# Performance work log

Hardware: AMD Instinct MI355X
Metric: run time of the kernel (lower is better)

## Reference

```python
import jax, jax.numpy as jnp
import numpy as np

B, H, KVH, HD, S = 16, 32, 8, 128, 4096
D = H * HD  # 4096
Q = 1  # decode: one query token per batch element


def rotate_half(x):
    half = x.shape[-1] // 2
    return jnp.concatenate([-x[..., half:], x[..., :half]], axis=-1)


def setup_inputs() -> dict:
    key = jax.random.key(0)
    ks = jax.random.split(key, 8)
    hidden_states = jax.random.normal(ks[0], (B, Q, D), dtype=jnp.float32)
    current_steps = jax.random.randint(ks[1], (B,), 0, S - 1)
    # additive causal mask per batch: positions <= current_step visible
    pos = jnp.arange(S)[None, :]
    attention_mask = jnp.where(pos <= current_steps[:, None], 0.0, -1e9).astype(jnp.float32)[:, None, None, :]  # [B,1,1,S]
    # RoPE cos/sin at each batch element's current position
    inv_freq = 1.0 / (10000.0 ** (jnp.arange(0, HD, 2, dtype=jnp.float32) / HD))
    ang = current_steps[:, None].astype(jnp.float32) * inv_freq[None, :]  # [B, HD/2]
    ang = jnp.concatenate([ang, ang], axis=-1)  # [B, HD]
    cos = jnp.cos(ang)[:, None, None, :]  # [B,1,1,HD]
    sin = jnp.sin(ang)[:, None, None, :]
    past_key = jax.random.normal(ks[2], (B, KVH, S, HD), dtype=jnp.float32)
    past_value = jax.random.normal(ks[3], (B, KVH, S, HD), dtype=jnp.float32)
    sc = 1.0 / np.sqrt(D)
    Wq = jax.random.normal(ks[4], (D, H * HD), dtype=jnp.float32) * sc
    Wk = jax.random.normal(ks[5], (D, KVH * HD), dtype=jnp.float32) * sc
    Wv = jax.random.normal(ks[6], (D, KVH * HD), dtype=jnp.float32) * sc
    Wo = jax.random.normal(ks[7], (H * HD, D), dtype=jnp.float32) * sc
    return dict(hidden_states=hidden_states, attention_mask=attention_mask,
                current_steps=current_steps, cos=cos, sin=sin,
                past_key=past_key, past_value=past_value,
                Wq=Wq, Wk=Wk, Wv=Wv, Wo=Wo)


def reference(hidden_states, attention_mask, current_steps, cos, sin,
              past_key, past_value, Wq, Wk, Wv, Wo):
    b, q_len, d = hidden_states.shape
    # projections -> [B, heads, Q, HD]
    q = (hidden_states @ Wq).reshape(b, q_len, H, HD).transpose(0, 2, 1, 3)
    k = (hidden_states @ Wk).reshape(b, q_len, KVH, HD).transpose(0, 2, 1, 3)
    v = (hidden_states @ Wv).reshape(b, q_len, KVH, HD).transpose(0, 2, 1, 3)
    # RoPE
    q = q * cos + rotate_half(q) * sin
    k = k * cos + rotate_half(k) * sin
    # KV-cache scatter at current_step per batch (slice_scatter equivalent)
    def upd(cache_b, new_b, step):
        return jax.lax.dynamic_update_slice(cache_b, new_b, (0, step, 0))
    new_key = jax.vmap(upd)(past_key, k, current_steps)      # [B,KVH,S,HD]
    new_value = jax.vmap(upd)(past_value, v, current_steps)  # [B,KVH,S,HD]
    # GQA attention
    g = H // KVH
    qg = q.reshape(b, KVH, g, q_len, HD)
    scores = jnp.einsum('bkgqd,bksd->bkgqs', qg, new_key) / np.sqrt(HD)
    scores = scores + attention_mask[:, :, None, :, :]  # [B,1,1,Q,S] broadcast
    probs = jax.nn.softmax(scores, axis=-1)
    out = jnp.einsum('bkgqs,bksd->bkgqd', probs, new_value)
    out = out.reshape(b, H, q_len, HD).transpose(0, 2, 1, 3).reshape(b, q_len, H * HD)
    attn_out = out @ Wo
    return attn_out, new_key, new_value
```

## Files before the change

kernel.cpp:

```cpp
#include <hip/hip_runtime.h>

#define B 16
#define H 32
#define KVH 8
#define HD 128
#define S 4096
#define D 4096
#define NQKV 6144
#define PSPLIT 32
#define WSPLIT 32
#define NCH 16
#define CROWS (S / NCH)
#define SCALE 0.08838834764831845f

typedef float nfloat4 __attribute__((ext_vector_type(4)));

__device__ __forceinline__ float4 ntload4(const float4* p) {
  nfloat4 r = __builtin_nontemporal_load(reinterpret_cast<const nfloat4*>(p));
  return *reinterpret_cast<float4*>(&r);
}
__device__ __forceinline__ float ntloadf(const float* p) {
  return __builtin_nontemporal_load(p);
}

__global__ void k_proj(const float* __restrict__ hs, const float* __restrict__ Wq,
                       const float* __restrict__ Wk, const float* __restrict__ Wv,
                       float* __restrict__ part) {
  __shared__ float4 hsT[D / PSPLIT][4];
  int t = threadIdx.x;
  int n = blockIdx.x * 256 + t;
  int k0 = blockIdx.y * (D / PSPLIT);
#pragma unroll
  for (int i = 0; i < (D / PSPLIT) * 4 / 256; i++) {
    int idx = i * 256 + t;
    int k = idx >> 2, b4 = idx & 3;
    hsT[k][b4] = make_float4(hs[(size_t)(b4 * 4 + 0) * D + k0 + k],
                             hs[(size_t)(b4 * 4 + 1) * D + k0 + k],
                             hs[(size_t)(b4 * 4 + 2) * D + k0 + k],
                             hs[(size_t)(b4 * 4 + 3) * D + k0 + k]);
  }
  const float* w; int ldw, col;
  if (n < 4096)      { w = Wq; ldw = 4096; col = n; }
  else if (n < 5120) { w = Wk; ldw = 1024; col = n - 4096; }
  else               { w = Wv; ldw = 1024; col = n - 5120; }
  float acc[B];
#pragma unroll
  for (int b = 0; b < B; b++) acc[b] = 0.f;
  const float* wp = w + (size_t)k0 * ldw + col;
  __syncthreads();
#pragma unroll 4
  for (int k = 0; k < D / PSPLIT; k++) {
    float wv = ntloadf(&wp[(size_t)k * ldw]);
    float4 h0 = hsT[k][0], h1 = hsT[k][1], h2 = hsT[k][2], h3 = hsT[k][3];
    acc[0]  = fmaf(h0.x, wv, acc[0]);  acc[1]  = fmaf(h0.y, wv, acc[1]);
    acc[2]  = fmaf(h0.z, wv, acc[2]);  acc[3]  = fmaf(h0.w, wv, acc[3]);
    acc[4]  = fmaf(h1.x, wv, acc[4]);  acc[5]  = fmaf(h1.y, wv, acc[5]);
    acc[6]  = fmaf(h1.z, wv, acc[6]);  acc[7]  = fmaf(h1.w, wv, acc[7]);
    acc[8]  = fmaf(h2.x, wv, acc[8]);  acc[9]  = fmaf(h2.y, wv, acc[9]);
    acc[10] = fmaf(h2.z, wv, acc[10]); acc[11] = fmaf(h2.w, wv, acc[11]);
    acc[12] = fmaf(h3.x, wv, acc[12]); acc[13] = fmaf(h3.y, wv, acc[13]);
    acc[14] = fmaf(h3.z, wv, acc[14]); acc[15] = fmaf(h3.w, wv, acc[15]);
  }
  float* p = part + (size_t)blockIdx.y * (B * NQKV);
#pragma unroll
  for (int b = 0; b < B; b++) p[(size_t)b * NQKV + n] = acc[b];
}

__global__ void k_reduce_rope(const float* __restrict__ part, const float* __restrict__ cosb,
                              const float* __restrict__ sinb, const int* __restrict__ steps,
                              float* __restrict__ qr, float* __restrict__ nkrow,
                              float* __restrict__ nvrow) {
  int i = blockIdx.x * 256 + threadIdx.x;
  int b = i / 3584, n2 = i % 3584;
  if (n2 < 2560) {
    int hr = n2 >> 6, d = n2 & 63;
    int n_lo = hr * 128 + d, n_hi = n_lo + 64;
    float vlo = 0.f, vhi = 0.f;
#pragma unroll
    for (int c = 0; c < PSPLIT; c++) {
      const float* pc = part + (size_t)c * B * NQKV + (size_t)b * NQKV;
      vlo += ntloadf(&pc[n_lo]);
      vhi += ntloadf(&pc[n_hi]);
    }
    float clo = cosb[b * HD + d], chi = cosb[b * HD + d + 64];
    float slo = sinb[b * HD + d], shi = sinb[b * HD + d + 64];
    float rlo = vlo * clo - vhi * slo;
    float rhi = vhi * chi + vlo * shi;
    if (n_lo < 4096) {
      qr[(size_t)b * D + n_lo] = rlo;
      qr[(size_t)b * D + n_hi] = rhi;
    } else {
      nkrow[(size_t)b * KVH * HD + (n_lo - 4096)] = rlo;
      nkrow[(size_t)b * KVH * HD + (n_hi - 4096)] = rhi;
    }
  } else {
    int j = n2 - 2560;
    float v = 0.f;
#pragma unroll
    for (int c = 0; c < PSPLIT; c++)
      v += ntloadf(&part[(size_t)c * B * NQKV + (size_t)b * NQKV + 5120 + j]);
    nvrow[(size_t)b * KVH * HD + j] = v;
  }
}

__global__ void __launch_bounds__(256)
k_flashKV(const float* __restrict__ pastk, const float* __restrict__ pastv,
          const float* __restrict__ nkrow, const float* __restrict__ nvrow,
          const float* __restrict__ qr, const int* __restrict__ steps,
          float* __restrict__ newk, float* __restrict__ newv,
          float* __restrict__ part, float* __restrict__ stats) {
  int ch = blockIdx.x, kvh = blockIdx.y, b = blockIdx.z;
  int t = threadIdx.x;
  __shared__ float sbuf[CROWS][4];
  __shared__ float redmx[4][4];
  __shared__ float redsm[4][4];
  __shared__ float4 red4[4][4][32];
  int s0 = ch * CROWS;
  int step = steps[b];
  int L = step + 1;
  int h0 = kvh * 4;
  bool any = (s0 < L);
  int w = t >> 6;
  int d4 = t & 31, rr = t >> 5;

  const float4* srcv = (const float4*)(pastv + ((size_t)(b * KVH + kvh) * S + s0) * HD);
  float4*       dstv = (float4*)(newv + ((size_t)(b * KVH + kvh) * S + s0) * HD);
  float4 vsub = ((const float4*)(nvrow + (size_t)(b * KVH + kvh) * HD))[d4];

  {
    int ln = t & 15, rg = t >> 4;
    const float4* qbase = (const float4*)(qr + ((size_t)b * H + h0) * HD);
    float4 q0[4], q1[4];
#pragma unroll
    for (int h = 0; h < 4; h++) {
      q0[h] = qbase[h * 32 + ln];
      q1[h] = qbase[h * 32 + ln + 16];
    }
    const float4* subp = (const float4*)(nkrow + (size_t)(b * KVH + kvh) * HD);
    float4 sub0 = subp[ln], sub1 = subp[ln + 16];
    const float4* src = (const float4*)(pastk + ((size_t)(b * KVH + kvh) * S + s0) * HD);
    float4*       dst = (float4*)(newk + ((size_t)(b * KVH + kvh) * S + s0) * HD);
#pragma unroll 4
    for (int it = 0; it < CROWS / 16; ++it) {
      int row = it * 16 + rg;
      size_t o0 = (size_t)row * 32 + ln;
      float4 k0 = ntload4(&src[o0]);
      float4 k1 = ntload4(&src[o0 + 16]);
      if (s0 + row == step) { k0 = sub0; k1 = sub1; }
      dst[o0] = k0;
      dst[o0 + 16] = k1;
      if (s0 + it * 16 < L) {
        float a0, a1, a2, a3;
        a0 = fmaf(k0.x, q0[0].x, fmaf(k0.y, q0[0].y, fmaf(k0.z, q0[0].z, fmaf(k0.w, q0[0].w,
             fmaf(k1.x, q1[0].x, fmaf(k1.y, q1[0].y, fmaf(k1.z, q1[0].z, k1.w * q1[0].w)))))));
        a1 = fmaf(k0.x, q0[1].x, fmaf(k0.y, q0[1].y, fmaf(k0.z, q0[1].z, fmaf(k0.w, q0[1].w,
             fmaf(k1.x, q1[1].x, fmaf(k1.y, q1[1].y, fmaf(k1.z, q1[1].z, k1.w * q1[1].w)))))));
        a2 = fmaf(k0.x, q0[2].x, fmaf(k0.y, q0[2].y, fmaf(k0.z, q0[2].z, fmaf(k0.w, q0[2].w,
             fmaf(k1.x, q1[2].x, fmaf(k1.y, q1[2].y, fmaf(k1.z, q1[2].z, k1.w * q1[2].w)))))));
        a3 = fmaf(k0.x, q0[3].x, fmaf(k0.y, q0[3].y, fmaf(k0.z, q0[3].z, fmaf(k0.w, q0[3].w,
             fmaf(k1.x, q1[3].x, fmaf(k1.y, q1[3].y, fmaf(k1.z, q1[3].z, k1.w * q1[3].w)))))));
#pragma unroll
        for (int o = 1; o < 16; o <<= 1) {
          a0 += __shfl_xor(a0, o);
          a1 += __shfl_xor(a1, o);
          a2 += __shfl_xor(a2, o);
          a3 += __shfl_xor(a3, o);
        }
        if (ln < 4) {
          float my = (ln == 0) ? a0 : (ln == 1) ? a1 : (ln == 2) ? a2 : a3;
          sbuf[row][ln] = my * SCALE;
        }
      }
    }
  }
  float4 pv0 = ntload4(&srcv[(size_t)rr * 32 + d4]);
  float4 pv1 = ntload4(&srcv[(size_t)(rr + 8) * 32 + d4]);
  __syncthreads();

  bool valid = any && (s0 + t < L);
  float s_0 = valid ? sbuf[t][0] : -1e30f;
  float s_1 = valid ? sbuf[t][1] : -1e30f;
  float s_2 = valid ? sbuf[t][2] : -1e30f;
  float s_3 = valid ? sbuf[t][3] : -1e30f;
  float mx0 = s_0, mx1 = s_1, mx2 = s_2, mx3 = s_3;
#pragma unroll
  for (int o = 1; o < 64; o <<= 1) {
    mx0 = fmaxf(mx0, __shfl_xor(mx0, o));
    mx1 = fmaxf(mx1, __shfl_xor(mx1, o));
    mx2 = fmaxf(mx2, __shfl_xor(mx2, o));
    mx3 = fmaxf(mx3, __shfl_xor(mx3, o));
  }
  if ((t & 63) == 0) { redmx[w][0] = mx0; redmx[w][1] = mx1; redmx[w][2] = mx2; redmx[w][3] = mx3; }
  __syncthreads();
  float m0 = fmaxf(fmaxf(redmx[0][0], redmx[1][0]), fmaxf(redmx[2][0], redmx[3][0]));
  float m1 = fmaxf(fmaxf(redmx[0][1], redmx[1][1]), fmaxf(redmx[2][1], redmx[3][1]));
  float m2 = fmaxf(fmaxf(redmx[0][2], redmx[1][2]), fmaxf(redmx[2][2], redmx[3][2]));
  float m3 = fmaxf(fmaxf(redmx[0][3], redmx[1][3]), fmaxf(redmx[2][3], redmx[3][3]));
  float e0 = valid ? __expf(s_0 - m0) : 0.f;
  float e1 = valid ? __expf(s_1 - m1) : 0.f;
  float e2 = valid ? __expf(s_2 - m2) : 0.f;
  float e3 = valid ? __expf(s_3 - m3) : 0.f;
  float es0 = e0, es1 = e1, es2 = e2, es3 = e3;
#pragma unroll
  for (int o = 1; o < 64; o <<= 1) {
    es0 += __shfl_xor(es0, o);
    es1 += __shfl_xor(es1, o);
    es2 += __shfl_xor(es2, o);
    es3 += __shfl_xor(es3, o);
  }
  if ((t & 63) == 0) { redsm[w][0] = es0; redsm[w][1] = es1; redsm[w][2] = es2; redsm[w][3] = es3; }
  sbuf[t][0] = e0; sbuf[t][1] = e1; sbuf[t][2] = e2; sbuf[t][3] = e3;
  __syncthreads();
  float l0 = redsm[0][0] + redsm[1][0] + redsm[2][0] + redsm[3][0];
  float l1 = redsm[0][1] + redsm[1][1] + redsm[2][1] + redsm[3][1];
  float l2 = redsm[0][2] + redsm[1][2] + redsm[2][2] + redsm[3][2];
  float l3 = redsm[0][3] + redsm[1][3] + redsm[2][3] + redsm[3][3];

  float4 a0 = make_float4(0.f, 0.f, 0.f, 0.f), a1 = a0, a2 = a0, a3 = a0;
#pragma unroll 2
  for (int i = 0; i < CROWS / 16; ++i) {
    int r0 = i * 16 + rr, r1 = r0 + 8;
    float4 v0 = pv0, v1 = pv1;
    if (i + 1 < CROWS / 16) {
      pv0 = ntload4(&srcv[(size_t)(r0 + 16) * 32 + d4]);
      pv1 = ntload4(&srcv[(size_t)(r1 + 16) * 32 + d4]);
    }
    if (s0 + r0 == step) v0 = vsub;
    if (s0 + r1 == step) v1 = vsub;
    dstv[(size_t)r0 * 32 + d4] = v0;
    dstv[(size_t)r1 * 32 + d4] = v1;
    if (any && i * 16 < L - s0) {
      float p00 = sbuf[r0][0], p01 = sbuf[r0][1], p02 = sbuf[r0][2], p03 = sbuf[r0][3];
      float p10 = sbuf[r1][0], p11 = sbuf[r1][1], p12 = sbuf[r1][2], p13 = sbuf[r1][3];
      a0.x = fmaf(p00, v0.x, fmaf(p10, v1.x, a0.x));
      a0.y = fmaf(p00, v0.y, fmaf(p10, v1.y, a0.y));
      a0.z = fmaf(p00, v0.z, fmaf(p10, v1.z, a0.z));
      a0.w = fmaf(p00, v0.w, fmaf(p10, v1.w, a0.w));
      a1.x = fmaf(p01, v0.x, fmaf(p11, v1.x, a1.x));
      a1.y = fmaf(p01, v0.y, fmaf(p11, v1.y, a1.y));
      a1.z = fmaf(p01, v0.z, fmaf(p11, v1.z, a1.z));
      a1.w = fmaf(p01, v0.w, fmaf(p11, v1.w, a1.w));
      a2.x = fmaf(p02, v0.x, fmaf(p12, v1.x, a2.x));
      a2.y = fmaf(p02, v0.y, fmaf(p12, v1.y, a2.y));
      a2.z = fmaf(p02, v0.z, fmaf(p12, v1.z, a2.z));
      a2.w = fmaf(p02, v0.w, fmaf(p12, v1.w, a2.w));
      a3.x = fmaf(p03, v0.x, fmaf(p13, v1.x, a3.x));
      a3.y = fmaf(p03, v0.y, fmaf(p13, v1.y, a3.y));
      a3.z = fmaf(p03, v0.z, fmaf(p13, v1.z, a3.z));
      a3.w = fmaf(p03, v0.w, fmaf(p13, v1.w, a3.w));
    }
  }
  a0.x += __shfl_xor(a0.x, 32); a0.y += __shfl_xor(a0.y, 32);
  a0.z += __shfl_xor(a0.z, 32); a0.w += __shfl_xor(a0.w, 32);
  a1.x += __shfl_xor(a1.x, 32); a1.y += __shfl_xor(a1.y, 32);
  a1.z += __shfl_xor(a1.z, 32); a1.w += __shfl_xor(a1.w, 32);
  a2.x += __shfl_xor(a2.x, 32); a2.y += __shfl_xor(a2.y, 32);
  a2.z += __shfl_xor(a2.z, 32); a2.w += __shfl_xor(a2.w, 32);
  a3.x += __shfl_xor(a3.x, 32); a3.y += __shfl_xor(a3.y, 32);
  a3.z += __shfl_xor(a3.z, 32); a3.w += __shfl_xor(a3.w, 32);
  if ((t & 32) == 0) {
    red4[w][0][d4] = a0; red4[w][1][d4] = a1; red4[w][2][d4] = a2; red4[w][3][d4] = a3;
  }
  __syncthreads();
  if (t < 128) {
    int hh = t >> 5, dd = t & 31;
    float4 x0 = red4[0][hh][dd], x1 = red4[1][hh][dd], x2 = red4[2][hh][dd], x3 = red4[3][hh][dd];
    float4 s;
    s.x = (x0.x + x1.x) + (x2.x + x3.x);
    s.y = (x0.y + x1.y) + (x2.y + x3.y);
    s.z = (x0.z + x1.z) + (x2.z + x3.z);
    s.w = (x0.w + x1.w) + (x2.w + x3.w);
    ((float4*)(part + (((size_t)ch * B + b) * KVH + kvh) * 512))[t] = s;
  }
  if (t == 0) {
    size_t si = (((size_t)ch * B + b) * KVH + kvh) * 8;
    stats[si + 0] = m0; stats[si + 1] = l0;
    stats[si + 2] = m1; stats[si + 3] = l1;
    stats[si + 4] = m2; stats[si + 5] = l2;
    stats[si + 6] = m3; stats[si + 7] = l3;
  }
}

__global__ void k_reduce_ctx(const float* __restrict__ part, const float* __restrict__ stats,
                             float* __restrict__ ctx) {
  int i = blockIdx.x * 256 + threadIdx.x;
  int b = i >> 12, r = i & 4095, h = r >> 7, d = r & 127;
  int kvh = h >> 2, hl = h & 3;
  float M = -1e30f;
#pragma unroll
  for (int c = 0; c < NCH; c++)
    M = fmaxf(M, stats[(((size_t)c * B + b) * KVH + kvh) * 8 + hl * 2]);
  float num = 0.f, den = 0.f;
#pragma unroll
  for (int c = 0; c < NCH; c++) {
    size_t si = (((size_t)c * B + b) * KVH + kvh) * 8 + hl * 2;
    float wgt = __expf(stats[si] - M);
    den += wgt * stats[si + 1];
    num += wgt * ntloadf(&part[(((size_t)c * B + b) * KVH + kvh) * 512 + hl * 128 + d]);
  }
  ctx[i] = num / den;
}

__global__ void k_wo(const float* __restrict__ ctx, const float* __restrict__ Wo,
                     float* __restrict__ part) {
  __shared__ float4 cxT[D / WSPLIT][4];
  int t = threadIdx.x;
  int n = blockIdx.x * 256 + t;
  int k0 = blockIdx.y * (D / WSPLIT);
#pragma unroll
  for (int i = 0; i < (D / WSPLIT) * 4 / 256; i++) {
    int idx = i * 256 + t;
    int k = idx >> 2, b4 = idx & 3;
    cxT[k][b4] = make_float4(ctx[(size_t)(b4 * 4 + 0) * D + k0 + k],
                             ctx[(size_t)(b4 * 4 + 1) * D + k0 + k],
                             ctx[(size_t)(b4 * 4 + 2) * D + k0 + k],
                             ctx[(size_t)(b4 * 4 + 3) * D + k0 + k]);
  }
  float acc[B];
#pragma unroll
  for (int b = 0; b < B; b++) acc[b] = 0.f;
  const float* wp = Wo + (size_t)k0 * D + n;
  __syncthreads();
#pragma unroll 4
  for (int k = 0; k < D / WSPLIT; k++) {
    float wv = ntloadf(&wp[(size_t)k * D]);
    float4 h0 = cxT[k][0], h1 = cxT[k][1], h2 = cxT[k][2], h3 = cxT[k][3];
    acc[0]  = fmaf(h0.x, wv, acc[0]);  acc[1]  = fmaf(h0.y, wv, acc[1]);
    acc[2]  = fmaf(h0.z, wv, acc[2]);  acc[3]  = fmaf(h0.w, wv, acc[3]);
    acc[4]  = fmaf(h1.x, wv, acc[4]);  acc[5]  = fmaf(h1.y, wv, acc[5]);
    acc[6]  = fmaf(h1.z, wv, acc[6]);  acc[7]  = fmaf(h1.w, wv, acc[7]);
    acc[8]  = fmaf(h2.x, wv, acc[8]);  acc[9]  = fmaf(h2.y, wv, acc[9]);
    acc[10] = fmaf(h2.z, wv, acc[10]); acc[11] = fmaf(h2.w, wv, acc[11]);
    acc[12] = fmaf(h3.x, wv, acc[12]); acc[13] = fmaf(h3.y, wv, acc[13]);
    acc[14] = fmaf(h3.z, wv, acc[14]); acc[15] = fmaf(h3.w, wv, acc[15]);
  }
  float* p = part + (size_t)blockIdx.y * (B * D);
#pragma unroll
  for (int b = 0; b < B; b++) p[(size_t)b * D + n] = acc[b];
}

__global__ void k_reduce_out(const float* __restrict__ part, float* __restrict__ out) {
  int i = blockIdx.x * 256 + threadIdx.x;
  float s = 0.f;
#pragma unroll
  for (int c = 0; c < WSPLIT; c++) s += ntloadf(&part[(size_t)c * B * D + i]);
  out[i] = s;
}

extern "C" void kernel_launch(void* const* d_in, const int* in_sizes, int n_in,
                              void* d_out, int out_size, void* d_ws, size_t ws_size,
                              hipStream_t stream) {
  const float* hs    = (const float*)d_in[0];
  const int*   steps = (const int*)d_in[2];
  const float* cosb  = (const float*)d_in[3];
  const float* sinb  = (const float*)d_in[4];
  const float* pk    = (const float*)d_in[5];
  const float* pvv   = (const float*)d_in[6];
  const float* Wq    = (const float*)d_in[7];
  const float* Wk    = (const float*)d_in[8];
  const float* Wv    = (const float*)d_in[9];
  const float* Wo    = (const float*)d_in[10];

  float* attn_out = (float*)d_out;
  float* newk = attn_out + (size_t)B * D;
  float* newv = newk + (size_t)B * KVH * S * HD;

  float* ws = (float*)d_ws;
  float* A        = ws;
  float* p_part   = A;
  float* p_wopart = A;
  float* p_pvpart = A + 3145728;
  float* p_stats  = p_pvpart + 1048576;
  float* p_qr     = p_stats + 16384;
  float* p_nkrow  = p_qr + (size_t)B * D;
  float* p_nvrow  = p_nkrow + (size_t)B * KVH * HD;
  float* p_ctx    = p_nvrow + (size_t)B * KVH * HD;

  hipLaunchKernelGGL(k_proj, dim3(NQKV / 256, PSPLIT), dim3(256), 0, stream,
                     hs, Wq, Wk, Wv, p_part);
  hipLaunchKernelGGL(k_reduce_rope, dim3(B * 3584 / 256), dim3(256), 0, stream,
                     p_part, cosb, sinb, steps, p_qr, p_nkrow, p_nvrow);
  hipLaunchKernelGGL(k_flashKV, dim3(NCH, KVH, B), dim3(256), 0, stream,
                     pk, pvv, p_nkrow, p_nvrow, p_qr, steps, newk, newv,
                     p_pvpart, p_stats);
  hipLaunchKernelGGL(k_reduce_ctx, dim3(B * D / 256), dim3(256), 0, stream,
                     p_pvpart, p_stats, p_ctx);
  hipLaunchKernelGGL(k_wo, dim3(D / 256, WSPLIT), dim3(256), 0, stream,
                     p_ctx, Wo, p_wopart);
  hipLaunchKernelGGL(k_reduce_out, dim3(B * D / 256), dim3(256), 0, stream,
                     p_wopart, attn_out);
}
```

Baseline: 291.2 us.

## Make each wavefront own its 64 KV rows with a per-wave softmax

Each 64-lane wavefront now handles its own contiguous 64-row slice of the chunk for K scoring, softmax, and the V accumulation. The per-wave max and sum are combined at the end with an online-softmax rescale. This removes three block-wide barriers between the QK, softmax, and PV phases, so waves proceed independently and the score buffer becomes wave-private. It also lets fully masked waves skip compute at a finer grain, at the cost of extra exps in the final merge and a shallower per-thread V prefetch.

```diff
diff --git a/kernel.cpp b/kernel.cpp
--- a/kernel.cpp
+++ b/kernel.cpp
@@ -111,24 +111,23 @@
           float* __restrict__ part, float* __restrict__ stats) {
   int ch = blockIdx.x, kvh = blockIdx.y, b = blockIdx.z;
   int t = threadIdx.x;
-  __shared__ float sbuf[CROWS][4];
-  __shared__ float redmx[4][4];
-  __shared__ float redsm[4][4];
+  int w = t >> 6, lam = t & 63;
+  __shared__ float4 sbufv[4][64];
+  __shared__ float redm[4][4];
+  __shared__ float redl[4][4];
   __shared__ float4 red4[4][4][32];
   int s0 = ch * CROWS;
   int step = steps[b];
   int L = step + 1;
   int h0 = kvh * 4;
-  bool any = (s0 < L);
-  int w = t >> 6;
-  int d4 = t & 31, rr = t >> 5;
-
+  int rbase = s0 + w * 64;
+  const float4* srck = (const float4*)(pastk + ((size_t)(b * KVH + kvh) * S + s0) * HD);
   const float4* srcv = (const float4*)(pastv + ((size_t)(b * KVH + kvh) * S + s0) * HD);
-  float4*       dstv = (float4*)(newv + ((size_t)(b * KVH + kvh) * S + s0) * HD);
-  float4 vsub = ((const float4*)(nvrow + (size_t)(b * KVH + kvh) * HD))[d4];
+  float4* dstk = (float4*)(newk + ((size_t)(b * KVH + kvh) * S + s0) * HD);
+  float4* dstv = (float4*)(newv + ((size_t)(b * KVH + kvh) * S + s0) * HD);
 
   {
-    int ln = t & 15, rg = t >> 4;
+    int ln = lam & 15, rg = lam >> 4;
     const float4* qbase = (const float4*)(qr + ((size_t)b * H + h0) * HD);
     float4 q0[4], q1[4];
 #pragma unroll
@@ -138,18 +137,16 @@
     }
     const float4* subp = (const float4*)(nkrow + (size_t)(b * KVH + kvh) * HD);
     float4 sub0 = subp[ln], sub1 = subp[ln + 16];
-    const float4* src = (const float4*)(pastk + ((size_t)(b * KVH + kvh) * S + s0) * HD);
-    float4*       dst = (float4*)(newk + ((size_t)(b * KVH + kvh) * S + s0) * HD);
 #pragma unroll 4
-    for (int it = 0; it < CROWS / 16; ++it) {
-      int row = it * 16 + rg;
-      size_t o0 = (size_t)row * 32 + ln;
-      float4 k0 = ntload4(&src[o0]);
-      float4 k1 = ntload4(&src[o0 + 16]);
-      if (s0 + row == step) { k0 = sub0; k1 = sub1; }
-      dst[o0] = k0;
-      dst[o0 + 16] = k1;
-      if (s0 + it * 16 < L) {
+    for (int it = 0; it < 16; ++it) {
+      int rl = w * 64 + it * 4 + rg;
+      size_t o0 = (size_t)rl * 32 + ln;
+      float4 k0 = ntload4(&srck[o0]);
+      float4 k1 = ntload4(&srck[o0 + 16]);
+      if (s0 + rl == step) { k0 = sub0; k1 = sub1; }
+      dstk[o0] = k0;
+      dstk[o0 + 16] = k1;
+      if (rbase + it * 4 < L) {
         float a0, a1, a2, a3;
         a0 = fmaf(k0.x, q0[0].x, fmaf(k0.y, q0[0].y, fmaf(k0.z, q0[0].z, fmaf(k0.w, q0[0].w,
              fmaf(k1.x, q1[0].x, fmaf(k1.y, q1[0].y, fmaf(k1.z, q1[0].z, k1.w * q1[0].w)))))));
@@ -168,86 +165,61 @@
         }
         if (ln < 4) {
           float my = (ln == 0) ? a0 : (ln == 1) ? a1 : (ln == 2) ? a2 : a3;
-          sbuf[row][ln] = my * SCALE;
+          ((float*)&sbufv[w][it * 4 + rg])[ln] = my * SCALE;
         }
       }
     }
   }
-  float4 pv0 = ntload4(&srcv[(size_t)rr * 32 + d4]);
-  float4 pv1 = ntload4(&srcv[(size_t)(rr + 8) * 32 + d4]);
-  __syncthreads();
-
-  bool valid = any && (s0 + t < L);
-  float s_0 = valid ? sbuf[t][0] : -1e30f;
-  float s_1 = valid ? sbuf[t][1] : -1e30f;
-  float s_2 = valid ? sbuf[t][2] : -1e30f;
-  float s_3 = valid ? sbuf[t][3] : -1e30f;
-  float mx0 = s_0, mx1 = s_1, mx2 = s_2, mx3 = s_3;
+  int d4 = lam & 31, rv = lam >> 5;
+  float4 pv = ntload4(&srcv[(size_t)(w * 64 + rv) * 32 + d4]);
+  float4 vsub = ((const float4*)(nvrow + (size_t)(b * KVH + kvh) * HD))[d4];
+
+  bool valid = (rbase + lam < L);
+  float4 sc = sbufv[w][lam];
+  float s_0 = valid ? sc.x : -1e30f;
+  float s_1 = valid ? sc.y : -1e30f;
+  float s_2 = valid ? sc.z : -1e30f;
+  float s_3 = valid ? sc.w : -1e30f;
+  float m0 = s_0, m1 = s_1, m2 = s_2, m3 = s_3;
 #pragma unroll
   for (int o = 1; o < 64; o <<= 1) {
-    mx0 = fmaxf(mx0, __shfl_xor(mx0, o));
-    mx1 = fmaxf(mx1, __shfl_xor(mx1, o));
-    mx2 = fmaxf(mx2, __shfl_xor(mx2, o));
-    mx3 = fmaxf(mx3, __shfl_xor(mx3, o));
-  }
-  if ((t & 63) == 0) { redmx[w][0] = mx0; redmx[w][1] = mx1; redmx[w][2] = mx2; redmx[w][3] = mx3; }
-  __syncthreads();
-  float m0 = fmaxf(fmaxf(redmx[0][0], redmx[1][0]), fmaxf(redmx[2][0], redmx[3][0]));
-  float m1 = fmaxf(fmaxf(redmx[0][1], redmx[1][1]), fmaxf(redmx[2][1], redmx[3][1]));
-  float m2 = fmaxf(fmaxf(redmx[0][2], redmx[1][2]), fmaxf(redmx[2][2], redmx[3][2]));
-  float m3 = fmaxf(fmaxf(redmx[0][3], redmx[1][3]), fmaxf(redmx[2][3], redmx[3][3]));
+    m0 = fmaxf(m0, __shfl_xor(m0, o));
+    m1 = fmaxf(m1, __shfl_xor(m1, o));
+    m2 = fmaxf(m2, __shfl_xor(m2, o));
+    m3 = fmaxf(m3, __shfl_xor(m3, o));
+  }
   float e0 = valid ? __expf(s_0 - m0) : 0.f;
   float e1 = valid ? __expf(s_1 - m1) : 0.f;
   float e2 = valid ? __expf(s_2 - m2) : 0.f;
   float e3 = valid ? __expf(s_3 - m3) : 0.f;
-  float es0 = e0, es1 = e1, es2 = e2, es3 = e3;
+  float l0 = e0, l1 = e1, l2 = e2, l3 = e3;
 #pragma unroll
   for (int o = 1; o < 64; o <<= 1) {
-    es0 += __shfl_xor(es0, o);
-    es1 += __shfl_xor(es1, o);
-    es2 += __shfl_xor(es2, o);
-    es3 += __shfl_xor(es3, o);
-  }
-  if ((t & 63) == 0) { redsm[w][0] = es0; redsm[w][1] = es1; redsm[w][2] = es2; redsm[w][3] = es3; }
-  sbuf[t][0] = e0; sbuf[t][1] = e1; sbuf[t][2] = e2; sbuf[t][3] = e3;
-  __syncthreads();
-  float l0 = redsm[0][0] + redsm[1][0] + redsm[2][0] + redsm[3][0];
-  float l1 = redsm[0][1] + redsm[1][1] + redsm[2][1] + redsm[3][1];
-  float l2 = redsm[0][2] + redsm[1][2] + redsm[2][2] + redsm[3][2];
-  float l3 = redsm[0][3] + redsm[1][3] + redsm[2][3] + redsm[3][3];
+    l0 += __shfl_xor(l0, o);
+    l1 += __shfl_xor(l1, o);
+    l2 += __shfl_xor(l2, o);
+    l3 += __shfl_xor(l3, o);
+  }
+  sbufv[w][lam] = make_float4(e0, e1, e2, e3);
 
   float4 a0 = make_float4(0.f, 0.f, 0.f, 0.f), a1 = a0, a2 = a0, a3 = a0;
-#pragma unroll 2
-  for (int i = 0; i < CROWS / 16; ++i) {
-    int r0 = i * 16 + rr, r1 = r0 + 8;
-    float4 v0 = pv0, v1 = pv1;
-    if (i + 1 < CROWS / 16) {
-      pv0 = ntload4(&srcv[(size_t)(r0 + 16) * 32 + d4]);
-      pv1 = ntload4(&srcv[(size_t)(r1 + 16) * 32 + d4]);
-    }
-    if (s0 + r0 == step) v0 = vsub;
-    if (s0 + r1 == step) v1 = vsub;
-    dstv[(size_t)r0 * 32 + d4] = v0;
-    dstv[(size_t)r1 * 32 + d4] = v1;
-    if (any && i * 16 < L - s0) {
-      float p00 = sbuf[r0][0], p01 = sbuf[r0][1], p02 = sbuf[r0][2], p03 = sbuf[r0][3];
-      float p10 = sbuf[r1][0], p11 = sbuf[r1][1], p12 = sbuf[r1][2], p13 = sbuf[r1][3];
-      a0.x = fmaf(p00, v0.x, fmaf(p10, v1.x, a0.x));
-      a0.y = fmaf(p00, v0.y, fmaf(p10, v1.y, a0.y));
-      a0.z = fmaf(p00, v0.z, fmaf(p10, v1.z, a0.z));
-      a0.w = fmaf(p00, v0.w, fmaf(p10, v1.w, a0.w));
-      a1.x = fmaf(p01, v0.x, fmaf(p11, v1.x, a1.x));
-      a1.y = fmaf(p01, v0.y, fmaf(p11, v1.y, a1.y));
-      a1.z = fmaf(p01, v0.z, fmaf(p11, v1.z, a1.z));
-      a1.w = fmaf(p01, v0.w, fmaf(p11, v1.w, a1.w));
-      a2.x = fmaf(p02, v0.x, fmaf(p12, v1.x, a2.x));
-      a2.y = fmaf(p02, v0.y, fmaf(p12, v1.y, a2.y));
-      a2.z = fmaf(p02, v0.z, fmaf(p12, v1.z, a2.z));
-      a2.w = fmaf(p02, v0.w, fmaf(p12, v1.w, a2.w));
-      a3.x = fmaf(p03, v0.x, fmaf(p13, v1.x, a3.x));
-      a3.y = fmaf(p03, v0.y, fmaf(p13, v1.y, a3.y));
-      a3.z = fmaf(p03, v0.z, fmaf(p13, v1.z, a3.z));
-      a3.w = fmaf(p03, v0.w, fmaf(p13, v1.w, a3.w));
+#pragma unroll 4
+  for (int i = 0; i < 32; ++i) {
+    int rl = w * 64 + i * 2 + rv;
+    float4 v = pv;
+    if (i < 31) pv = ntload4(&srcv[(size_t)(rl + 2) * 32 + d4]);
+    if (s0 + rl == step) v = vsub;
+    dstv[(size_t)rl * 32 + d4] = v;
+    if (rbase + i * 2 < L) {
+      float4 p4 = sbufv[w][i * 2 + rv];
+      a0.x = fmaf(p4.x, v.x, a0.x); a0.y = fmaf(p4.x, v.y, a0.y);
+      a0.z = fmaf(p4.x, v.z, a0.z); a0.w = fmaf(p4.x, v.w, a0.w);
+      a1.x = fmaf(p4.y, v.x, a1.x); a1.y = fmaf(p4.y, v.y, a1.y);
+      a1.z = fmaf(p4.y, v.z, a1.z); a1.w = fmaf(p4.y, v.w, a1.w);
+      a2.x = fmaf(p4.z, v.x, a2.x); a2.y = fmaf(p4.z, v.y, a2.y);
+      a2.z = fmaf(p4.z, v.z, a2.z); a2.w = fmaf(p4.z, v.w, a2.w);
+      a3.x = fmaf(p4.w, v.x, a3.x); a3.y = fmaf(p4.w, v.y, a3.y);
+      a3.z = fmaf(p4.w, v.z, a3.z); a3.w = fmaf(p4.w, v.w, a3.w);
     }
   }
   a0.x += __shfl_xor(a0.x, 32); a0.y += __shfl_xor(a0.y, 32);
@@ -258,26 +230,35 @@
   a2.z += __shfl_xor(a2.z, 32); a2.w += __shfl_xor(a2.w, 32);
   a3.x += __shfl_xor(a3.x, 32); a3.y += __shfl_xor(a3.y, 32);
   a3.z += __shfl_xor(a3.z, 32); a3.w += __shfl_xor(a3.w, 32);
-  if ((t & 32) == 0) {
-    red4[w][0][d4] = a0; red4[w][1][d4] = a1; red4[w][2][d4] = a2; red4[w][3][d4] = a3;
+  if (lam < 32) {
+    red4[w][0][lam] = a0; red4[w][1][lam] = a1;
+    red4[w][2][lam] = a2; red4[w][3][lam] = a3;
+  }
+  if (lam == 0) {
+    redm[w][0] = m0; redm[w][1] = m1; redm[w][2] = m2; redm[w][3] = m3;
+    redl[w][0] = l0; redl[w][1] = l1; redl[w][2] = l2; redl[w][3] = l3;
   }
   __syncthreads();
+
   if (t < 128) {
     int hh = t >> 5, dd = t & 31;
+    float mw0 = redm[0][hh], mw1 = redm[1][hh], mw2 = redm[2][hh], mw3 = redm[3][hh];
+    float mc = fmaxf(fmaxf(mw0, mw1), fmaxf(mw2, mw3));
+    float g0 = __expf(mw0 - mc), g1 = __expf(mw1 - mc);
+    float g2 = __expf(mw2 - mc), g3 = __expf(mw3 - mc);
     float4 x0 = red4[0][hh][dd], x1 = red4[1][hh][dd], x2 = red4[2][hh][dd], x3 = red4[3][hh][dd];
     float4 s;
-    s.x = (x0.x + x1.x) + (x2.x + x3.x);
-    s.y = (x0.y + x1.y) + (x2.y + x3.y);
-    s.z = (x0.z + x1.z) + (x2.z + x3.z);
-    s.w = (x0.w + x1.w) + (x2.w + x3.w);
+    s.x = g0 * x0.x + g1 * x1.x + g2 * x2.x + g3 * x3.x;
+    s.y = g0 * x0.y + g1 * x1.y + g2 * x2.y + g3 * x3.y;
+    s.z = g0 * x0.z + g1 * x1.z + g2 * x2.z + g3 * x3.z;
+    s.w = g0 * x0.w + g1 * x1.w + g2 * x2.w + g3 * x3.w;
     ((float4*)(part + (((size_t)ch * B + b) * KVH + kvh) * 512))[t] = s;
-  }
-  if (t == 0) {
-    size_t si = (((size_t)ch * B + b) * KVH + kvh) * 8;
-    stats[si + 0] = m0; stats[si + 1] = l0;
-    stats[si + 2] = m1; stats[si + 3] = l1;
-    stats[si + 4] = m2; stats[si + 5] = l2;
-    stats[si + 6] = m3; stats[si + 7] = l3;
+    if (dd == 0) {
+      float lc = g0 * redl[0][hh] + g1 * redl[1][hh] + g2 * redl[2][hh] + g3 * redl[3][hh];
+      size_t si = (((size_t)ch * B + b) * KVH + kvh) * 8;
+      stats[si + hh * 2] = mc;
+      stats[si + hh * 2 + 1] = lc;
+    }
   }
 }
 
```

After: 295.7 us. Within noise of the previous version (+1.5%).
